# Kernel optimization log

Hardware: AMD Instinct MI355X
Metric: run time of the kernel (lower is better)

The kernel has to match this reference:

```python
import jax, jax.numpy as jnp
import numpy as np


def setup_inputs() -> dict:
    key = jax.random.key(0)
    x = jax.random.normal(key, (64, 512, 16, 16), dtype=jnp.float32)
    return {"x": x}


def reference(x):
    # x: [B, dim, h, w] -> covariance pooling y: [B, dim, dim]
    B, dim, h, w = x.shape
    M = h * w
    xf = x.reshape(B, dim, M)
    # I_hat = (1/M) I - (1/M^2) 11^T  (centering matrix scaled by 1/M)
    inv_M = jnp.asarray(1.0 / M, dtype=x.dtype)
    I_hat = inv_M * jnp.eye(M, dtype=x.dtype) - (inv_M * inv_M) * jnp.ones((M, M), dtype=x.dtype)
    # y = x @ I_hat @ x^T, I_hat broadcast over batch
    xI = jnp.einsum('bdm,mn->bdn', xf, I_hat)   # [B, dim, M]
    y = jnp.einsum('bdn,ben->bde', xI, xf)      # [B, dim, dim]
    return y
```

## Files before the change

kernel.cpp:

```cpp
#include <hip/hip_runtime.h>
#include <stdint.h>


typedef __attribute__((ext_vector_type(8))) short bf16x8;
typedef __attribute__((ext_vector_type(4))) float f32x4;

static __device__ __forceinline__ unsigned short f2bf(float f) {
    union { float f; uint32_t u; } c; c.f = f;
    uint32_t u = c.u;
    return (unsigned short)((u + 0x7FFFu + ((u >> 16) & 1u)) >> 16);
}

static __device__ __forceinline__ void cvt_store(f32x4 v0, f32x4 v1, float* psum,
                                                 unsigned short* dst) {
    v0 *= 0.0625f; v1 *= 0.0625f;
    *psum += (v0.x + v0.y + v0.z + v0.w) + (v1.x + v1.y + v1.z + v1.w);
    bf16x8 o;
    o[0] = (short)f2bf(v0.x); o[1] = (short)f2bf(v0.y);
    o[2] = (short)f2bf(v0.z); o[3] = (short)f2bf(v0.w);
    o[4] = (short)f2bf(v1.x); o[5] = (short)f2bf(v1.y);
    o[6] = (short)f2bf(v1.z); o[7] = (short)f2bf(v1.w);
    *(bf16x8*)dst = o;
}

__global__ __launch_bounds__(512, 4) void covpool_fused(const float* __restrict__ x,
                                                        float* __restrict__ y) {
    __shared__ __align__(16) unsigned short As[128 * 32];
    __shared__ __align__(16) unsigned short Bs[128 * 32];
    __shared__ __align__(16) float Ep[32 * 132];
    __shared__ float muA[128];
    __shared__ float muB[128];

    const int xcd = blockIdx.x & 7;
    const int j   = blockIdx.x >> 3;
    const int b   = xcd * 8 + j / 10;
    const int t10 = j % 10;
    const unsigned code = (unsigned)((0xFBA7653210ULL >> (4 * t10)) & 15ULL);
    const int tm = code >> 2, tn = code & 3;
    const bool diag = (tm == tn);

    const float* Ag = x + ((size_t)b * 512 + tm * 128) * 256;
    const float* Bg = x + ((size_t)b * 512 + tn * 128) * 256;

    const int tid  = threadIdx.x;
    const int lane = tid & 63;
    const int wave = tid >> 6;
    const int wm = (wave >> 1) * 32;
    const int wn = (wave & 1) * 64;

    f32x4 acc[2][4] = {};
    float pA = 0.f, pB = 0.f;

    const int rl  = lane & 15;
    const int q   = lane >> 4;
    const int swl = (q ^ ((rl >> 1) & 3)) * 8;
    const int srow = tid >> 2, schunk = tid & 3;
    const int slot = schunk ^ ((srow >> 1) & 3);
    unsigned short* Adst = As + srow * 32 + slot * 8;
    unsigned short* Bdst = Bs + srow * 32 + slot * 8;
    const float* Asrc = Ag + (size_t)srow * 256 + schunk * 8;
    const float* Bsrc = Bg + (size_t)srow * 256 + schunk * 8;

    f32x4 a0, a1, b0, b1;
    a0 = *(const f32x4*)Asrc; a1 = *(const f32x4*)(Asrc + 4);
    if (!diag) { b0 = *(const f32x4*)Bsrc; b1 = *(const f32x4*)(Bsrc + 4); }

    for (int kk = 0; kk < 256; kk += 32) {
        __syncthreads();
        cvt_store(a0, a1, &pA, Adst);
        if (!diag) cvt_store(b0, b1, &pB, Bdst);
        __syncthreads();
        if (kk < 224) {
            a0 = *(const f32x4*)(Asrc + kk + 32);
            a1 = *(const f32x4*)(Asrc + kk + 36);
            if (!diag) {
                b0 = *(const f32x4*)(Bsrc + kk + 32);
                b1 = *(const f32x4*)(Bsrc + kk + 36);
            }
        }
        const unsigned short* Bsr = diag ? As : Bs;
        bf16x8 af[2], bfr[4];
#pragma unroll
        for (int i = 0; i < 2; ++i)
            af[i] = *(const bf16x8*)(As + (wm + i * 16 + rl) * 32 + swl);
#pragma unroll
        for (int jj = 0; jj < 4; ++jj)
            bfr[jj] = *(const bf16x8*)(Bsr + (wn + jj * 16 + rl) * 32 + swl);
#pragma unroll
        for (int i = 0; i < 2; ++i)
#pragma unroll
            for (int jj = 0; jj < 4; ++jj)
                acc[i][jj] = __builtin_amdgcn_mfma_f32_16x16x32_bf16(
                    af[i], bfr[jj], acc[i][jj], 0, 0, 0);
    }

    {
        float s = pA;
        s += __shfl_xor(s, 1, 64); s += __shfl_xor(s, 2, 64);
        if (schunk == 0) muA[srow] = s * 0.0625f;
        if (!diag) {
            float sb = pB;
            sb += __shfl_xor(sb, 1, 64); sb += __shfl_xor(sb, 2, 64);
            if (schunk == 0) muB[srow] = sb * 0.0625f;
        }
    }
    const float* muBp = diag ? muA : muB;
    float* yb = y + (size_t)b * 512 * 512;

#pragma unroll
    for (int c = 0; c < 4; ++c) {
        __syncthreads();
        if ((wave >> 1) == c) {
#pragma unroll
            for (int i = 0; i < 2; ++i) {
#pragma unroll
                for (int jj = 0; jj < 4; ++jj) {
                    const int col = wn + jj * 16 + rl;
                    const float mb = muBp[col];
#pragma unroll
                    for (int r = 0; r < 4; ++r) {
                        const int row = wm + i * 16 + q * 4 + r;
                        Ep[(i * 16 + q * 4 + r) * 132 + col] = acc[i][jj][r] - muA[row] * mb;
                    }
                }
            }
        }
        __syncthreads();
#pragma unroll
        for (int v = 0; v < 2; ++v) {
            const int flat = v * 512 + tid;
            const int rloc = flat >> 5, c4 = flat & 31;
            f32x4 val = *(const f32x4*)(Ep + rloc * 132 + c4 * 4);
            *(f32x4*)(yb + (size_t)(tm * 128 + c * 32 + rloc) * 512 + tn * 128 + c4 * 4) = val;
        }
        if (!diag) {
#pragma unroll
            for (int v = 0; v < 2; ++v) {
                const int id = v * 512 + tid;
                const int cc = id >> 3, g = id & 7;
                f32x4 val;
#pragma unroll
                for (int e = 0; e < 4; ++e)
                    val[e] = Ep[(g * 4 + e) * 132 + cc];
                *(f32x4*)(yb + (size_t)(tn * 128 + cc) * 512 + tm * 128 + c * 32 + g * 4) = val;
            }
        }
    }
}

extern "C" void kernel_launch(void* const* d_in, const int* in_sizes, int n_in,
                              void* d_out, int out_size, void* d_ws, size_t ws_size,
                              hipStream_t stream) {
    const float* x = (const float*)d_in[0];
    float* yout = (float*)d_out;
    (void)d_ws; (void)ws_size;
    covpool_fused<<<640, 512, 0, stream>>>(x, yout);
}
```

Measured before the change: 112.0 us.

## Split into bf16 prep kernel and LDS-free GEMM over full tile grid

Replaces the single fused kernel with two kernels. The first converts x to bf16 in a workspace and computes row means. The second runs the GEMM reading bf16 fragments straight from global memory without LDS, computing all 16 tiles per batch instead of exploiting symmetry, and writes results directly with nontemporal scalar stores. The intent is to remove repeated fp32 conversion, LDS staging and barriers. In exchange it adds an extra launch and a workspace round trip, duplicates the symmetric tiles, and issues uncoalesced scalar stores.

```diff
diff --git a/kernel.cpp b/kernel.cpp
--- a/kernel.cpp
+++ b/kernel.cpp
@@ -11,139 +11,98 @@
     return (unsigned short)((u + 0x7FFFu + ((u >> 16) & 1u)) >> 16);
 }
 
-static __device__ __forceinline__ void cvt_store(f32x4 v0, f32x4 v1, float* psum,
-                                                 unsigned short* dst) {
-    v0 *= 0.0625f; v1 *= 0.0625f;
-    *psum += (v0.x + v0.y + v0.z + v0.w) + (v1.x + v1.y + v1.z + v1.w);
-    bf16x8 o;
-    o[0] = (short)f2bf(v0.x); o[1] = (short)f2bf(v0.y);
-    o[2] = (short)f2bf(v0.z); o[3] = (short)f2bf(v0.w);
-    o[4] = (short)f2bf(v1.x); o[5] = (short)f2bf(v1.y);
-    o[6] = (short)f2bf(v1.z); o[7] = (short)f2bf(v1.w);
-    *(bf16x8*)dst = o;
+__global__ __launch_bounds__(256) void covpool_prep(const float* __restrict__ x,
+                                                    unsigned short* __restrict__ xbf,
+                                                    float* __restrict__ mu) {
+    const int blk = blockIdx.x;
+    const int xcd = blk & 7, r = blk >> 3;
+    const int b   = xcd * 8 + (r >> 4);
+    const int seg = r & 15;
+    const size_t rowbase = (size_t)b * 512 + seg * 32;
+    const float* xs = x + rowbase * 256;
+    unsigned short* xd = xbf + rowbase * 256;
+    const int tid = threadIdx.x;
+
+#pragma unroll
+    for (int it = 0; it < 4; ++it) {
+        const int cid = it * 256 + tid;
+        const int row = cid >> 5;
+        const int sub = cid & 31;
+        const float* g = xs + row * 256 + sub * 8;
+        f32x4 v0 = __builtin_nontemporal_load((const f32x4*)g);
+        f32x4 v1 = __builtin_nontemporal_load((const f32x4*)(g + 4));
+        float s = (v0.x + v0.y + v0.z + v0.w) + (v1.x + v1.y + v1.z + v1.w);
+        s += __shfl_xor(s, 1, 64);  s += __shfl_xor(s, 2, 64);
+        s += __shfl_xor(s, 4, 64);  s += __shfl_xor(s, 8, 64);
+        s += __shfl_xor(s, 16, 64);
+        bf16x8 o;
+        o[0] = (short)f2bf(v0.x); o[1] = (short)f2bf(v0.y);
+        o[2] = (short)f2bf(v0.z); o[3] = (short)f2bf(v0.w);
+        o[4] = (short)f2bf(v1.x); o[5] = (short)f2bf(v1.y);
+        o[6] = (short)f2bf(v1.z); o[7] = (short)f2bf(v1.w);
+        *(bf16x8*)(xd + row * 256 + sub * 8) = o;
+        if (sub == 0) mu[rowbase + row] = s * (1.0f / 256.0f);
+    }
 }
 
-__global__ __launch_bounds__(512, 4) void covpool_fused(const float* __restrict__ x,
-                                                        float* __restrict__ y) {
-    __shared__ __align__(16) unsigned short As[128 * 32];
-    __shared__ __align__(16) unsigned short Bs[128 * 32];
-    __shared__ __align__(16) float Ep[32 * 132];
-    __shared__ float muA[128];
-    __shared__ float muB[128];
-
-    const int xcd = blockIdx.x & 7;
-    const int j   = blockIdx.x >> 3;
-    const int b   = xcd * 8 + j / 10;
-    const int t10 = j % 10;
-    const unsigned code = (unsigned)((0xFBA7653210ULL >> (4 * t10)) & 15ULL);
-    const int tm = code >> 2, tn = code & 3;
-    const bool diag = (tm == tn);
-
-    const float* Ag = x + ((size_t)b * 512 + tm * 128) * 256;
-    const float* Bg = x + ((size_t)b * 512 + tn * 128) * 256;
+__global__ __launch_bounds__(256, 4) void covpool_gemm(const unsigned short* __restrict__ xbf,
+                                                       const float* __restrict__ mu,
+                                                       float* __restrict__ y) {
+    const int blk = blockIdx.x;
+    const int xcd = blk & 7, r = blk >> 3;
+    const int b   = xcd * 8 + (r >> 4);
+    const int t   = r & 15;
+    const int tm = t >> 2, tn = t & 3;
 
     const int tid  = threadIdx.x;
     const int lane = tid & 63;
     const int wave = tid >> 6;
-    const int wm = (wave >> 1) * 32;
+    const int wm = (wave >> 1) * 64;
     const int wn = (wave & 1) * 64;
+    const int rl = lane & 15;
+    const int q  = lane >> 4;
 
-    f32x4 acc[2][4] = {};
-    float pA = 0.f, pB = 0.f;
+    const unsigned short* Ap = xbf + ((size_t)b * 512 + tm * 128 + wm + rl) * 256 + q * 8;
+    const unsigned short* Bp = xbf + ((size_t)b * 512 + tn * 128 + wn + rl) * 256 + q * 8;
 
-    const int rl  = lane & 15;
-    const int q   = lane >> 4;
-    const int swl = (q ^ ((rl >> 1) & 3)) * 8;
-    const int srow = tid >> 2, schunk = tid & 3;
-    const int slot = schunk ^ ((srow >> 1) & 3);
-    unsigned short* Adst = As + srow * 32 + slot * 8;
-    unsigned short* Bdst = Bs + srow * 32 + slot * 8;
-    const float* Asrc = Ag + (size_t)srow * 256 + schunk * 8;
-    const float* Bsrc = Bg + (size_t)srow * 256 + schunk * 8;
-
-    f32x4 a0, a1, b0, b1;
-    a0 = *(const f32x4*)Asrc; a1 = *(const f32x4*)(Asrc + 4);
-    if (!diag) { b0 = *(const f32x4*)Bsrc; b1 = *(const f32x4*)(Bsrc + 4); }
-
-    for (int kk = 0; kk < 256; kk += 32) {
-        __syncthreads();
-        cvt_store(a0, a1, &pA, Adst);
-        if (!diag) cvt_store(b0, b1, &pB, Bdst);
-        __syncthreads();
-        if (kk < 224) {
-            a0 = *(const f32x4*)(Asrc + kk + 32);
-            a1 = *(const f32x4*)(Asrc + kk + 36);
-            if (!diag) {
-                b0 = *(const f32x4*)(Bsrc + kk + 32);
-                b1 = *(const f32x4*)(Bsrc + kk + 36);
-            }
-        }
-        const unsigned short* Bsr = diag ? As : Bs;
-        bf16x8 af[2], bfr[4];
+    f32x4 acc[4][4] = {};
 #pragma unroll
-        for (int i = 0; i < 2; ++i)
-            af[i] = *(const bf16x8*)(As + (wm + i * 16 + rl) * 32 + swl);
+    for (int kk = 0; kk < 8; ++kk) {
+        bf16x8 af[4], bfr[4];
+#pragma unroll
+        for (int i = 0; i < 4; ++i)
+            af[i] = *(const bf16x8*)(Ap + (size_t)i * 16 * 256 + kk * 32);
 #pragma unroll
         for (int jj = 0; jj < 4; ++jj)
-            bfr[jj] = *(const bf16x8*)(Bsr + (wn + jj * 16 + rl) * 32 + swl);
+            bfr[jj] = *(const bf16x8*)(Bp + (size_t)jj * 16 * 256 + kk * 32);
 #pragma unroll
-        for (int i = 0; i < 2; ++i)
+        for (int i = 0; i < 4; ++i)
 #pragma unroll
             for (int jj = 0; jj < 4; ++jj)
                 acc[i][jj] = __builtin_amdgcn_mfma_f32_16x16x32_bf16(
                     af[i], bfr[jj], acc[i][jj], 0, 0, 0);
     }
 
-    {
-        float s = pA;
-        s += __shfl_xor(s, 1, 64); s += __shfl_xor(s, 2, 64);
-        if (schunk == 0) muA[srow] = s * 0.0625f;
-        if (!diag) {
-            float sb = pB;
-            sb += __shfl_xor(sb, 1, 64); sb += __shfl_xor(sb, 2, 64);
-            if (schunk == 0) muB[srow] = sb * 0.0625f;
-        }
-    }
-    const float* muBp = diag ? muA : muB;
+    const float* muR = mu + b * 512 + tm * 128 + wm;
+    const float* muC = mu + b * 512 + tn * 128 + wn;
+    f32x4 ma[4];
+#pragma unroll
+    for (int i = 0; i < 4; ++i)
+        ma[i] = *(const f32x4*)(muR + i * 16 + q * 4);
+
     float* yb = y + (size_t)b * 512 * 512;
-
+    const float inv256 = 1.0f / 256.0f;
 #pragma unroll
-    for (int c = 0; c < 4; ++c) {
-        __syncthreads();
-        if ((wave >> 1) == c) {
+    for (int jj = 0; jj < 4; ++jj) {
+        const float mb = muC[jj * 16 + rl];
 #pragma unroll
-            for (int i = 0; i < 2; ++i) {
+        for (int i = 0; i < 4; ++i) {
+            const size_t rbase = (size_t)(tm * 128 + wm + i * 16 + q * 4) * 512
+                               + tn * 128 + wn + jj * 16 + rl;
 #pragma unroll
-                for (int jj = 0; jj < 4; ++jj) {
-                    const int col = wn + jj * 16 + rl;
-                    const float mb = muBp[col];
-#pragma unroll
-                    for (int r = 0; r < 4; ++r) {
-                        const int row = wm + i * 16 + q * 4 + r;
-                        Ep[(i * 16 + q * 4 + r) * 132 + col] = acc[i][jj][r] - muA[row] * mb;
-                    }
-                }
-            }
-        }
-        __syncthreads();
-#pragma unroll
-        for (int v = 0; v < 2; ++v) {
-            const int flat = v * 512 + tid;
-            const int rloc = flat >> 5, c4 = flat & 31;
-            f32x4 val = *(const f32x4*)(Ep + rloc * 132 + c4 * 4);
-            *(f32x4*)(yb + (size_t)(tm * 128 + c * 32 + rloc) * 512 + tn * 128 + c4 * 4) = val;
-        }
-        if (!diag) {
-#pragma unroll
-            for (int v = 0; v < 2; ++v) {
-                const int id = v * 512 + tid;
-                const int cc = id >> 3, g = id & 7;
-                f32x4 val;
-#pragma unroll
-                for (int e = 0; e < 4; ++e)
-                    val[e] = Ep[(g * 4 + e) * 132 + cc];
-                *(f32x4*)(yb + (size_t)(tn * 128 + cc) * 512 + tm * 128 + c * 32 + g * 4) = val;
-            }
+            for (int rr = 0; rr < 4; ++rr)
+                __builtin_nontemporal_store(acc[i][jj][rr] * inv256 - ma[i][rr] * mb,
+                                            yb + rbase + (size_t)rr * 512);
         }
     }
 }
@@ -153,6 +112,9 @@
                               hipStream_t stream) {
     const float* x = (const float*)d_in[0];
     float* yout = (float*)d_out;
-    (void)d_ws; (void)ws_size;
-    covpool_fused<<<640, 512, 0, stream>>>(x, yout);
+    unsigned short* xbf = (unsigned short*)d_ws;
+    float* mu = (float*)((char*)d_ws + (size_t)64 * 512 * 256 * 2);
+    (void)ws_size; (void)in_sizes; (void)n_in; (void)out_size;
+    covpool_prep<<<1024, 256, 0, stream>>>(x, xbf, mu);
+    covpool_gemm<<<1024, 256, 0, stream>>>(xbf, mu, yout);
 }
```

Result: slower. 127.1 us (+13.5%).
